# Kernel tuning notes

Measured on AMD Instinct MI355X. Metric: run time of the kernel, lower is better.

The kernel has to match this reference:

```python
import jax, jax.numpy as jnp
import numpy as np

N = 100_000   # nodes
E = 3_200_000 # edges
F = 13        # input features
H = 64        # hidden dim
G = 512       # graphs in batch
C = 2         # output classes
BN_EPS = 1e-5


def _linear(key, fan_in, fan_out):
    kw, kb = jax.random.split(key)
    bound = 1.0 / np.sqrt(fan_in)
    W = jax.random.uniform(kw, (fan_in, fan_out), jnp.float32, -bound, bound)
    b = jax.random.uniform(kb, (fan_out,), jnp.float32, -bound, bound)
    return W, b


def _conv_params(key, fin, fout):
    k1, k2, k3 = jax.random.split(key, 3)
    W1, b1 = _linear(k1, fin, fout)
    W2, b2 = _linear(k2, fout, fout)
    gamma = jnp.ones((fout,), jnp.float32)
    beta = jnp.zeros((fout,), jnp.float32)
    mean = jax.random.normal(k3, (fout,), jnp.float32) * 0.1
    var = jnp.ones((fout,), jnp.float32)
    return W1, b1, gamma, beta, mean, var, W2, b2


def setup_inputs() -> dict:
    key = jax.random.key(0)
    ks = jax.random.split(key, 10)
    x = jax.random.normal(ks[0], (N, F), jnp.float32)
    src = jax.random.randint(ks[1], (E,), 0, N, jnp.int32)
    dst = jax.random.randint(ks[2], (E,), 0, N, jnp.int32)
    batch = jnp.sort(jax.random.randint(ks[3], (N,), 0, G, jnp.int32))
    inp = {"x": x, "src": src, "dst": dst, "batch": batch}
    for i, name in enumerate(["c1", "c2", "c3"]):
        fin = F if i == 0 else H
        W1, b1, g, be, m, v, W2, b2 = _conv_params(ks[4 + i], fin, H)
        inp.update({f"{name}_W1": W1, f"{name}_b1": b1, f"{name}_g": g,
                    f"{name}_be": be, f"{name}_m": m, f"{name}_v": v,
                    f"{name}_W2": W2, f"{name}_b2": b2})
    inp["fc1_W"], inp["fc1_b"] = _linear(ks[7], 3 * H, 3 * H)
    inp["fc2_W"], inp["fc2_b"] = _linear(ks[8], 3 * H, C)
    return inp


def _mlp(h, W1, b1, g, be, m, v, W2, b2):
    # Linear -> BatchNorm1d (inference, running stats) -> ReLU -> Linear -> ReLU
    h = h @ W1 + b1
    h = (h - m) * jax.lax.rsqrt(v + BN_EPS) * g + be
    h = jax.nn.relu(h)
    return jax.nn.relu(h @ W2 + b2)


def _gin_conv(x, src, dst, mlp_params):
    # GINConv with eps=0: MLP(x + sum_{j->i} x_j) via scatter-add over edges
    agg = jax.ops.segment_sum(x[src], dst, num_segments=N)
    return _mlp(x + agg, *mlp_params)


def reference(x, src, dst, batch,
              c1_W1, c1_b1, c1_g, c1_be, c1_m, c1_v, c1_W2, c1_b2,
              c2_W1, c2_b1, c2_g, c2_be, c2_m, c2_v, c2_W2, c2_b2,
              c3_W1, c3_b1, c3_g, c3_be, c3_m, c3_v, c3_W2, c3_b2,
              fc1_W, fc1_b, fc2_W, fc2_b):
    h1 = jax.nn.relu(_gin_conv(x, src, dst, (c1_W1, c1_b1, c1_g, c1_be, c1_m, c1_v, c1_W2, c1_b2)))
    h2 = jax.nn.relu(_gin_conv(h1, src, dst, (c2_W1, c2_b1, c2_g, c2_be, c2_m, c2_v, c2_W2, c2_b2)))
    h3 = jax.nn.relu(_gin_conv(h2, src, dst, (c3_W1, c3_b1, c3_g, c3_be, c3_m, c3_v, c3_W2, c3_b2)))
    p1 = jax.ops.segment_sum(h1, batch, num_segments=G)
    p2 = jax.ops.segment_sum(h2, batch, num_segments=G)
    p3 = jax.ops.segment_sum(h3, batch, num_segments=G)
    h = jnp.concatenate([p1, p2, p3], axis=1)  # [G, 3H]
    h = jax.nn.relu(h @ fc1_W + fc1_b)
    # Dropout is identity in eval mode
    h = h @ fc2_W + fc2_b
    return jax.nn.log_softmax(h, axis=-1)
```

## Files before the change

### kernel.cpp

```cpp
#include <hip/hip_runtime.h>

#define NNODES 100000
#define NEDGES 3200000
#define NF 13
#define NFP 16
#define NG 512
#define BN_EPS 1e-5f
#define NTILES (NNODES / 16)
#define CAP 72

#define BSH 9
#define NBUCK ((NNODES + 511) / 512)
#define RCAP 18500
#define PTILE 4096
#define NPBLK ((NEDGES + PTILE - 1) / PTILE)
#define CVTB 200

#define NCHUNK ((NNODES + 63) / 64)
#define NPTASK (3 * NCHUNK)

typedef __attribute__((ext_vector_type(8))) _Float16 f16x8;
typedef __attribute__((ext_vector_type(4))) _Float16 f16x4;
typedef __attribute__((ext_vector_type(4))) float f32x4;

__device__ __forceinline__ unsigned short f2h(float f) {
    union { _Float16 h; unsigned short u; } c;
    c.h = (_Float16)f;
    return c.u;
}
__device__ __forceinline__ float h2f(unsigned short u) {
    union { _Float16 h; unsigned short u; } c;
    c.u = u;
    return (float)c.h;
}

__device__ __forceinline__ f16x8 shfl_xor8(f16x8 v, int m) {
    union { f16x8 h; int i[4]; } a, b;
    a.h = v;
#pragma unroll
    for (int k = 0; k < 4; ++k) b.i[k] = __shfl_xor(a.i[k], m, 64);
    return b.h;
}
__device__ __forceinline__ f16x4 shfl_xor4(f16x4 v, int m) {
    union { f16x4 h; int i[2]; } a, b;
    a.h = v;
#pragma unroll
    for (int k = 0; k < 2; ++k) b.i[k] = __shfl_xor(a.i[k], m, 64);
    return b.h;
}

__launch_bounds__(256)
__global__ void prep_kernel(const int* __restrict__ src, const int* __restrict__ dst,
                            int* __restrict__ gcount, int* __restrict__ pairbuf,
                            const float* __restrict__ x, unsigned short* __restrict__ xh,
                            const float* __restrict__ w10, const float* __restrict__ w20,
                            const float* __restrict__ w11, const float* __restrict__ w21,
                            const float* __restrict__ w12, const float* __restrict__ w22,
                            unsigned short* __restrict__ wfrag) {
    __shared__ int lhist[NBUCK];
    __shared__ int lbase[NBUCK];
    __shared__ int lpos[NBUCK];
    int bid = blockIdx.x;
    int t = threadIdx.x;

    if (bid < NPBLK) {
        int base = bid * PTILE;
        int cnt = NEDGES - base; if (cnt > PTILE) cnt = PTILE;
        int v[PTILE / 256], b[PTILE / 256];
#pragma unroll
        for (int j = 0; j < PTILE / 256; ++j) {
            int i = t + j * 256;
            if (i < cnt) {
                int d = __builtin_nontemporal_load(dst + base + i);
                int s = __builtin_nontemporal_load(src + base + i);
                b[j] = d >> BSH;
                v[j] = ((d & 511) << 17) | s;
            } else b[j] = -1;
        }
        if (t < NBUCK) lhist[t] = 0;
        __syncthreads();
#pragma unroll
        for (int j = 0; j < PTILE / 256; ++j)
            if (b[j] >= 0) atomicAdd(&lhist[b[j]], 1);
        __syncthreads();
        if (t < NBUCK) {
            lbase[t] = atomicAdd(&gcount[t], lhist[t]);
            lpos[t] = 0;
        }
        __syncthreads();
#pragma unroll
        for (int j = 0; j < PTILE / 256; ++j) {
            if (b[j] >= 0) {
                int p = atomicAdd(&lpos[b[j]], 1);
                pairbuf[(size_t)b[j] * RCAP + lbase[b[j]] + p] = v[j];
            }
        }
    } else if (bid < NPBLK + 12) {
        int tid = (bid - NPBLK) * 256 + t;
        if (tid >= 3072) return;
        int layer = tid >> 10;
        int rem = tid & 1023;
        int mat = rem >> 9;
        int tile = (rem >> 7) & 3;
        int chunk = (rem >> 6) & 1;
        int lane = rem & 63;
        int quad = lane >> 4, n = lane & 15;
        const float* W = (layer == 0) ? (mat ? w20 : w10)
                       : (layer == 1) ? (mat ? w21 : w11)
                                      : (mat ? w22 : w12);
        int K = (layer == 0 && mat == 0) ? NF : 64;
        unsigned short* o = wfrag + ((size_t)tid) * 8;
#pragma unroll
        for (int j = 0; j < 8; ++j) {
            int k = chunk * 32 + quad * 8 + j;
            float val = (k < K) ? W[k * 64 + tile * 16 + n] : 0.f;
            o[j] = f2h(val);
        }
    } else {
        const int total = NNODES * NFP;
        int idx = (bid - NPBLK - 12) * 256 + t;
        int stride = CVTB * 256;
        for (int i = idx; i < total; i += stride) {
            int n = i >> 4;
            int f = i & 15;
            xh[i] = (f < NF) ? f2h(__builtin_nontemporal_load(x + n * NF + f))
                             : (unsigned short)0;
        }
    }
}

__launch_bounds__(512)
__global__ void bucket_scatter_kernel(const int* __restrict__ pairbuf,
                                      const int* __restrict__ gcount,
                                      int* __restrict__ cursor, int* __restrict__ csr) {
    __shared__ int lcnt[512];
    int bk = blockIdx.x;
    int lo = bk << BSH;
    int cnt = gcount[bk];
    if (threadIdx.x < 512) lcnt[threadIdx.x] = 0;
    __syncthreads();
    const int* pb = pairbuf + (size_t)bk * RCAP;
    for (int i = threadIdx.x; i < cnt; i += 512) {
        int p = __builtin_nontemporal_load(pb + i);
        int s = p & 0x1FFFF;
        int dl = p >> 17;
        int pos = atomicAdd(&lcnt[dl], 1);
        csr[(size_t)(lo + dl) * CAP + pos] = s;
    }
    __syncthreads();
    int n = lo + threadIdx.x;
    if (threadIdx.x < 512 && n < NNODES) cursor[n] = n * CAP + lcnt[threadIdx.x];
}

template <int LAYER>
__launch_bounds__(256, 6)
__global__ void gin_layer_kernel(const unsigned short* __restrict__ xin,
                                 const int* __restrict__ cursor,
                                 const int* __restrict__ csr,
                                 const unsigned short* __restrict__ wfrag,
                                 const float* __restrict__ b1, const float* __restrict__ gam,
                                 const float* __restrict__ be, const float* __restrict__ mu,
                                 const float* __restrict__ var, const float* __restrict__ b2,
                                 unsigned short* __restrict__ hout) {
    constexpr int FSTR = (LAYER == 1) ? NFP : 64;
    __shared__ __align__(16) unsigned short ytile[16][80];
    __shared__ __align__(16) unsigned short ztile[16][80];
    int lane = threadIdx.x & 63;
    int wid = threadIdx.x >> 6;
    int quad = lane >> 4, n16 = lane & 15;
    int nb = blockIdx.x * 16;

    if constexpr (LAYER == 1) {
        int g = lane >> 2;
        int r = lane & 3;
#pragma unroll
        for (int pp = 0; pp < 2; ++pp) {
            int lnA = wid * 4 + pp * 2;
            int nA = nb + lnA, nB = nA + 1;
            int jA = nA * CAP, jB = nB * CAP;
            int endA = __builtin_nontemporal_load(cursor + nA);
            int endB = __builtin_nontemporal_load(cursor + nB);
            f16x4 accA = {0, 0, 0, 0};
            f16x4 accB = {0, 0, 0, 0};
            if (g == 0) {
                accA = *(const f16x4*)&xin[(size_t)nA * FSTR + r * 4];
                accB = *(const f16x4*)&xin[(size_t)nB * FSTR + r * 4];
            }
            while (jA + 16 <= endA && jB + 16 <= endB) {
                int iA = __builtin_nontemporal_load(csr + jA + g);
                int iB = __builtin_nontemporal_load(csr + jB + g);
                f16x4 vA = *(const f16x4*)&xin[(size_t)iA * FSTR + r * 4];
                f16x4 vB = *(const f16x4*)&xin[(size_t)iB * FSTR + r * 4];
                accA += vA; accB += vB;
                jA += 16; jB += 16;
            }
            for (; jA + 32 <= endA; jA += 32) {
                int i0 = __builtin_nontemporal_load(csr + jA + g);
                int i1 = __builtin_nontemporal_load(csr + jA + 16 + g);
                f16x4 v0 = *(const f16x4*)&xin[(size_t)i0 * FSTR + r * 4];
                f16x4 v1 = *(const f16x4*)&xin[(size_t)i1 * FSTR + r * 4];
                accA += v0; accA += v1;
            }
            for (; jA < endA; jA += 16) {
                int e = jA + g;
                if (e < endA) {
                    int i0 = __builtin_nontemporal_load(csr + e);
                    accA += *(const f16x4*)&xin[(size_t)i0 * FSTR + r * 4];
                }
            }
            for (; jB + 32 <= endB; jB += 32) {
                int i0 = __builtin_nontemporal_load(csr + jB + g);
                int i1 = __builtin_nontemporal_load(csr + jB + 16 + g);
                f16x4 v0 = *(const f16x4*)&xin[(size_t)i0 * FSTR + r * 4];
                f16x4 v1 = *(const f16x4*)&xin[(size_t)i1 * FSTR + r * 4];
                accB += v0; accB += v1;
            }
            for (; jB < endB; jB += 16) {
                int e = jB + g;
                if (e < endB) {
                    int i0 = __builtin_nontemporal_load(csr + e);
                    accB += *(const f16x4*)&xin[(size_t)i0 * FSTR + r * 4];
                }
            }
#pragma unroll
            for (int m = 4; m < 64; m <<= 1) {
                accA += shfl_xor4(accA, m);
                accB += shfl_xor4(accB, m);
            }
            if (g == 0) {
                *(f16x4*)&ytile[lnA][r * 4] = accA;
                *(f16x4*)&ytile[lnA + 1][r * 4] = accB;
            } else if (g == 1) {
                f16x4 z = {0, 0, 0, 0};
                *(f16x4*)&ytile[lnA][16 + r * 4] = z;
                *(f16x4*)&ytile[lnA + 1][16 + r * 4] = z;
            }
        }
    } else {
        int g = lane >> 3;
        int r = lane & 7;
#pragma unroll
        for (int pp = 0; pp < 2; ++pp) {
            int lnA = wid * 4 + pp * 2;
            int nA = nb + lnA, nB = nA + 1;
            int jA = nA * CAP, jB = nB * CAP;
            int endA = __builtin_nontemporal_load(cursor + nA);
            int endB = __builtin_nontemporal_load(cursor + nB);
            f16x8 accA = {0, 0, 0, 0, 0, 0, 0, 0};
            f16x8 accB = {0, 0, 0, 0, 0, 0, 0, 0};
            if (g == 0) {
                accA = *(const f16x8*)&xin[(size_t)nA * 64 + r * 8];
                accB = *(const f16x8*)&xin[(size_t)nB * 64 + r * 8];
            }
            while (jA + 16 <= endA && jB + 16 <= endB) {
                int iA0 = __builtin_nontemporal_load(csr + jA + g);
                int iA1 = __builtin_nontemporal_load(csr + jA + 8 + g);
                int iB0 = __builtin_nontemporal_load(csr + jB + g);
                int iB1 = __builtin_nontemporal_load(csr + jB + 8 + g);
                f16x8 vA0 = *(const f16x8*)&xin[(size_t)iA0 * 64 + r * 8];
                f16x8 vA1 = *(const f16x8*)&xin[(size_t)iA1 * 64 + r * 8];
                f16x8 vB0 = *(const f16x8*)&xin[(size_t)iB0 * 64 + r * 8];
                f16x8 vB1 = *(const f16x8*)&xin[(size_t)iB1 * 64 + r * 8];
                accA += vA0; accA += vA1;
                accB += vB0; accB += vB1;
                jA += 16; jB += 16;
            }
            for (; jA + 16 <= endA; jA += 16) {
                int i0 = __builtin_nontemporal_load(csr + jA + g);
                int i1 = __builtin_nontemporal_load(csr + jA + 8 + g);
                f16x8 v0 = *(const f16x8*)&xin[(size_t)i0 * 64 + r * 8];
                f16x8 v1 = *(const f16x8*)&xin[(size_t)i1 * 64 + r * 8];
                accA += v0; accA += v1;
            }
            for (; jA < endA; jA += 8) {
                int e = jA + g;
                if (e < endA) {
                    int i0 = __builtin_nontemporal_load(csr + e);
                    accA += *(const f16x8*)&xin[(size_t)i0 * 64 + r * 8];
                }
            }
            for (; jB + 16 <= endB; jB += 16) {
                int i0 = __builtin_nontemporal_load(csr + jB + g);
                int i1 = __builtin_nontemporal_load(csr + jB + 8 + g);
                f16x8 v0 = *(const f16x8*)&xin[(size_t)i0 * 64 + r * 8];
                f16x8 v1 = *(const f16x8*)&xin[(size_t)i1 * 64 + r * 8];
                accB += v0; accB += v1;
            }
            for (; jB < endB; jB += 8) {
                int e = jB + g;
                if (e < endB) {
                    int i0 = __builtin_nontemporal_load(csr + e);
                    accB += *(const f16x8*)&xin[(size_t)i0 * 64 + r * 8];
                }
            }
#pragma unroll
            for (int m = 8; m < 64; m <<= 1) {
                accA += shfl_xor8(accA, m);
                accB += shfl_xor8(accB, m);
            }
            if (g == 0) {
                *(f16x8*)&ytile[lnA][r * 8] = accA;
                *(f16x8*)&ytile[lnA + 1][r * 8] = accB;
            }
        }
    }

    const f16x8* wf = (const f16x8*)wfrag;
    f16x8 w1f0 = wf[((0 * 4 + wid) * 2 + 0) * 64 + lane];
    f16x8 w1f1 = (LAYER == 2) ? wf[((0 * 4 + wid) * 2 + 1) * 64 + lane] : w1f0;
    f16x8 w2f0 = wf[((1 * 4 + wid) * 2 + 0) * 64 + lane];
    f16x8 w2f1 = wf[((1 * 4 + wid) * 2 + 1) * 64 + lane];
    int f = wid * 16 + n16;
    float sc = gam[f] * rsqrtf(var[f] + BN_EPS);
    float sh = (b1[f] - mu[f]) * sc + be[f];
    float bb2 = b2[f];

    __syncthreads();

    f16x8 a0 = *(const f16x8*)&ytile[n16][quad * 8];
    f32x4 z4 = {0.f, 0.f, 0.f, 0.f};
    z4 = __builtin_amdgcn_mfma_f32_16x16x32_f16(a0, w1f0, z4, 0, 0, 0);
    if constexpr (LAYER == 2) {
        f16x8 a1 = *(const f16x8*)&ytile[n16][32 + quad * 8];
        z4 = __builtin_amdgcn_mfma_f32_16x16x32_f16(a1, w1f1, z4, 0, 0, 0);
    }
#pragma unroll
    for (int reg = 0; reg < 4; ++reg) {
        float z = fmaxf(fmaf(z4[reg], sc, sh), 0.f);
        ztile[quad * 4 + reg][wid * 16 + n16] = f2h(z);
    }
    __syncthreads();

    f16x8 az0 = *(const f16x8*)&ztile[n16][quad * 8];
    f16x8 az1 = *(const f16x8*)&ztile[n16][32 + quad * 8];
    f32x4 h4 = {0.f, 0.f, 0.f, 0.f};
    h4 = __builtin_amdgcn_mfma_f32_16x16x32_f16(az0, w2f0, h4, 0, 0, 0);
    h4 = __builtin_amdgcn_mfma_f32_16x16x32_f16(az1, w2f1, h4, 0, 0, 0);
#pragma unroll
    for (int reg = 0; reg < 4; ++reg) {
        float h = fmaxf(h4[reg] + bb2, 0.f);
        hout[(size_t)(nb + quad * 4 + reg) * 64 + wid * 16 + n16] = f2h(h);
    }
}

__launch_bounds__(256)
__global__ void pool_kernel(const unsigned short* __restrict__ h1,
                            const unsigned short* __restrict__ h2,
                            const unsigned short* __restrict__ h3,
                            const int* __restrict__ batch,
                            float* __restrict__ pool) {
    int task = blockIdx.x * 4 + (threadIdx.x >> 6);
    if (task >= NPTASK) return;
    int lane = threadIdx.x & 63;
    int layer = task / NCHUNK;
    int c = task - layer * NCHUNK;
    int n0 = c * 64;
    int n1 = n0 + 64; if (n1 > NNODES) n1 = NNODES;
    const unsigned short* hb = (layer == 0) ? h1 : (layer == 1) ? h2 : h3;
    float acc = 0.f;
    int curg = batch[n0];
    for (int n = n0; n < n1; ++n) {
        int gid = batch[n];
        if (gid != curg) {
            atomicAdd(&pool[(size_t)curg * 192 + layer * 64 + lane], acc);
            acc = 0.f;
            curg = gid;
        }
        acc += h2f(__builtin_nontemporal_load(hb + (size_t)n * 64 + lane));
    }
    atomicAdd(&pool[(size_t)curg * 192 + layer * 64 + lane], acc);
}

__global__ void head_kernel(const float* __restrict__ pool,
                            const float* __restrict__ fc1W, const float* __restrict__ fc1b,
                            const float* __restrict__ fc2W, const float* __restrict__ fc2b,
                            float* __restrict__ out) {
    __shared__ float ps[192];
    __shared__ float hs[192];
    int gi = blockIdx.x;
    int t = threadIdx.x;
    ps[t] = pool[gi * 192 + t];
    __syncthreads();
    float acc = fc1b[t];
#pragma unroll 8
    for (int k = 0; k < 192; ++k) acc = fmaf(ps[k], fc1W[k * 192 + t], acc);
    hs[t] = fmaxf(acc, 0.f);
    __syncthreads();
    if (t == 0) {
        float l0 = fc2b[0], l1 = fc2b[1];
        for (int k = 0; k < 192; ++k) {
            float h = hs[k];
            l0 = fmaf(h, fc2W[k * 2 + 0], l0);
            l1 = fmaf(h, fc2W[k * 2 + 1], l1);
        }
        float mx = fmaxf(l0, l1);
        float lse = mx + logf(expf(l0 - mx) + expf(l1 - mx));
        out[gi * 2 + 0] = l0 - lse;
        out[gi * 2 + 1] = l1 - lse;
    }
}

extern "C" void kernel_launch(void* const* d_in, const int* in_sizes, int n_in,
                              void* d_out, int out_size, void* d_ws, size_t ws_size,
                              hipStream_t stream) {
    const float* x = (const float*)d_in[0];
    const int* src = (const int*)d_in[1];
    const int* dst = (const int*)d_in[2];
    const int* batch = (const int*)d_in[3];
    const float* c1[8];
    const float* c2[8];
    const float* c3[8];
    for (int i = 0; i < 8; ++i) {
        c1[i] = (const float*)d_in[4 + i];
        c2[i] = (const float*)d_in[12 + i];
        c3[i] = (const float*)d_in[20 + i];
    }
    const float* fc1W = (const float*)d_in[28];
    const float* fc1b = (const float*)d_in[29];
    const float* fc2W = (const float*)d_in[30];
    const float* fc2b = (const float*)d_in[31];
    float* out = (float*)d_out;

    unsigned short* base = (unsigned short*)d_ws;
    const size_t NA = (size_t)NNODES * 64;
    unsigned short* xh  = base;
    unsigned short* h1  = xh + (size_t)NNODES * NFP;
    unsigned short* h2  = h1 + NA;
    unsigned short* h3  = h2 + NA;
    unsigned short* wfrag = h3 + NA;
    float* pool = (float*)(wfrag + 3 * 8192);
    int* ibase = (int*)(pool + (size_t)NG * 192);
    int* cursor  = ibase;
    int* gcount  = ibase + NNODES;
    int* csr     = gcount + NBUCK;
    int* pairbuf = csr + (size_t)NNODES * CAP + 256;

    hipMemsetAsync(gcount, 0, NBUCK * sizeof(int), stream);
    hipMemsetAsync(pool, 0, (size_t)NG * 192 * sizeof(float), stream);

    prep_kernel<<<NPBLK + 12 + CVTB, 256, 0, stream>>>(
        src, dst, gcount, pairbuf, x, xh,
        c1[0], c1[6], c2[0], c2[6], c3[0], c3[6], wfrag);
    bucket_scatter_kernel<<<NBUCK, 512, 0, stream>>>(pairbuf, gcount, cursor, csr);

    gin_layer_kernel<1><<<NTILES, 256, 0, stream>>>(
        xh, cursor, csr, wfrag + 0 * 8192,
        c1[1], c1[2], c1[3], c1[4], c1[5], c1[7], h1);
    gin_layer_kernel<2><<<NTILES, 256, 0, stream>>>(
        h1, cursor, csr, wfrag + 1 * 8192,
        c2[1], c2[2], c2[3], c2[4], c2[5], c2[7], h2);
    gin_layer_kernel<2><<<NTILES, 256, 0, stream>>>(
        h2, cursor, csr, wfrag + 2 * 8192,
        c3[1], c3[2], c3[3], c3[4], c3[5], c3[7], h3);

    pool_kernel<<<(NPTASK + 3) / 4, 256, 0, stream>>>(h1, h2, h3, batch, pool);
    head_kernel<<<NG, 192, 0, stream>>>(pool, fc1W, fc1b, fc2W, fc2b, out);
}
```

Before: 407.7 us.

## Replace two-pass bucketed CSR build with direct global-atomic slot insertion

Removes the bucket histogram/pairbuf pass and the per-bucket scatter kernel, and builds the fixed-capacity adjacency directly with one global atomicAdd per edge on a per-node counter. The GIN layers now read the degree count and clamp it to CAP instead of reading a precomputed cursor. It also lowers the launch-bounds occupancy hint from 6 to 4 waves. This trades one kernel and an intermediate buffer for 3.2M scattered global atomics, and it silently drops any edges beyond CAP per node.

```diff
diff --git a/kernel.cpp b/kernel.cpp
--- a/kernel.cpp
+++ b/kernel.cpp
@@ -9,13 +9,6 @@
 #define NTILES (NNODES / 16)
 #define CAP 72
 
-#define BSH 9
-#define NBUCK ((NNODES + 511) / 512)
-#define RCAP 18500
-#define PTILE 4096
-#define NPBLK ((NEDGES + PTILE - 1) / PTILE)
-#define CVTB 200
-
 #define NCHUNK ((NNODES + 63) / 64)
 #define NPTASK (3 * NCHUNK)
 
@@ -50,53 +43,29 @@
 }
 
 __launch_bounds__(256)
-__global__ void prep_kernel(const int* __restrict__ src, const int* __restrict__ dst,
-                            int* __restrict__ gcount, int* __restrict__ pairbuf,
-                            const float* __restrict__ x, unsigned short* __restrict__ xh,
+__global__ void build_csr_kernel(const int* __restrict__ src, const int* __restrict__ dst,
+                                 int* __restrict__ cnt, int* __restrict__ csr) {
+    int idx = blockIdx.x * blockDim.x + threadIdx.x;
+    int stride = gridDim.x * blockDim.x;
+    for (int e = idx; e < NEDGES; e += stride) {
+        int d = __builtin_nontemporal_load(dst + e);
+        int s = __builtin_nontemporal_load(src + e);
+        int pos = atomicAdd(&cnt[d], 1);
+        if (pos < CAP) csr[(size_t)d * CAP + pos] = s;
+    }
+}
+
+#define CVTB 200
+__launch_bounds__(256)
+__global__ void prep_kernel(const float* __restrict__ x, unsigned short* __restrict__ xh,
                             const float* __restrict__ w10, const float* __restrict__ w20,
                             const float* __restrict__ w11, const float* __restrict__ w21,
                             const float* __restrict__ w12, const float* __restrict__ w22,
                             unsigned short* __restrict__ wfrag) {
-    __shared__ int lhist[NBUCK];
-    __shared__ int lbase[NBUCK];
-    __shared__ int lpos[NBUCK];
     int bid = blockIdx.x;
     int t = threadIdx.x;
-
-    if (bid < NPBLK) {
-        int base = bid * PTILE;
-        int cnt = NEDGES - base; if (cnt > PTILE) cnt = PTILE;
-        int v[PTILE / 256], b[PTILE / 256];
-#pragma unroll
-        for (int j = 0; j < PTILE / 256; ++j) {
-            int i = t + j * 256;
-            if (i < cnt) {
-                int d = __builtin_nontemporal_load(dst + base + i);
-                int s = __builtin_nontemporal_load(src + base + i);
-                b[j] = d >> BSH;
-                v[j] = ((d & 511) << 17) | s;
-            } else b[j] = -1;
-        }
-        if (t < NBUCK) lhist[t] = 0;
-        __syncthreads();
-#pragma unroll
-        for (int j = 0; j < PTILE / 256; ++j)
-            if (b[j] >= 0) atomicAdd(&lhist[b[j]], 1);
-        __syncthreads();
-        if (t < NBUCK) {
-            lbase[t] = atomicAdd(&gcount[t], lhist[t]);
-            lpos[t] = 0;
-        }
-        __syncthreads();
-#pragma unroll
-        for (int j = 0; j < PTILE / 256; ++j) {
-            if (b[j] >= 0) {
-                int p = atomicAdd(&lpos[b[j]], 1);
-                pairbuf[(size_t)b[j] * RCAP + lbase[b[j]] + p] = v[j];
-            }
-        }
-    } else if (bid < NPBLK + 12) {
-        int tid = (bid - NPBLK) * 256 + t;
+    if (bid < 12) {
+        int tid = bid * 256 + t;
         if (tid >= 3072) return;
         int layer = tid >> 10;
         int rem = tid & 1023;
@@ -118,7 +87,7 @@
         }
     } else {
         const int total = NNODES * NFP;
-        int idx = (bid - NPBLK - 12) * 256 + t;
+        int idx = (bid - 12) * 256 + t;
         int stride = CVTB * 256;
         for (int i = idx; i < total; i += stride) {
             int n = i >> 4;
@@ -129,33 +98,10 @@
     }
 }
 
-__launch_bounds__(512)
-__global__ void bucket_scatter_kernel(const int* __restrict__ pairbuf,
-                                      const int* __restrict__ gcount,
-                                      int* __restrict__ cursor, int* __restrict__ csr) {
-    __shared__ int lcnt[512];
-    int bk = blockIdx.x;
-    int lo = bk << BSH;
-    int cnt = gcount[bk];
-    if (threadIdx.x < 512) lcnt[threadIdx.x] = 0;
-    __syncthreads();
-    const int* pb = pairbuf + (size_t)bk * RCAP;
-    for (int i = threadIdx.x; i < cnt; i += 512) {
-        int p = __builtin_nontemporal_load(pb + i);
-        int s = p & 0x1FFFF;
-        int dl = p >> 17;
-        int pos = atomicAdd(&lcnt[dl], 1);
-        csr[(size_t)(lo + dl) * CAP + pos] = s;
-    }
-    __syncthreads();
-    int n = lo + threadIdx.x;
-    if (threadIdx.x < 512 && n < NNODES) cursor[n] = n * CAP + lcnt[threadIdx.x];
-}
-
 template <int LAYER>
-__launch_bounds__(256, 6)
+__launch_bounds__(256, 4)
 __global__ void gin_layer_kernel(const unsigned short* __restrict__ xin,
-                                 const int* __restrict__ cursor,
+                                 const int* __restrict__ cnt,
                                  const int* __restrict__ csr,
                                  const unsigned short* __restrict__ wfrag,
                                  const float* __restrict__ b1, const float* __restrict__ gam,
@@ -177,9 +123,12 @@
         for (int pp = 0; pp < 2; ++pp) {
             int lnA = wid * 4 + pp * 2;
             int nA = nb + lnA, nB = nA + 1;
+            int dA = __builtin_nontemporal_load(cnt + nA);
+            int dB = __builtin_nontemporal_load(cnt + nB);
+            if (dA > CAP) dA = CAP;
+            if (dB > CAP) dB = CAP;
             int jA = nA * CAP, jB = nB * CAP;
-            int endA = __builtin_nontemporal_load(cursor + nA);
-            int endB = __builtin_nontemporal_load(cursor + nB);
+            int endA = jA + dA, endB = jB + dB;
             f16x4 accA = {0, 0, 0, 0};
             f16x4 accB = {0, 0, 0, 0};
             if (g == 0) {
@@ -243,9 +192,12 @@
         for (int pp = 0; pp < 2; ++pp) {
             int lnA = wid * 4 + pp * 2;
             int nA = nb + lnA, nB = nA + 1;
+            int dA = __builtin_nontemporal_load(cnt + nA);
+            int dB = __builtin_nontemporal_load(cnt + nB);
+            if (dA > CAP) dA = CAP;
+            if (dB > CAP) dB = CAP;
             int jA = nA * CAP, jB = nB * CAP;
-            int endA = __builtin_nontemporal_load(cursor + nA);
-            int endB = __builtin_nontemporal_load(cursor + nB);
+            int endA = jA + dA, endB = jB + dB;
             f16x8 accA = {0, 0, 0, 0, 0, 0, 0, 0};
             f16x8 accB = {0, 0, 0, 0, 0, 0, 0, 0};
             if (g == 0) {
@@ -430,27 +382,24 @@
     unsigned short* wfrag = h3 + NA;
     float* pool = (float*)(wfrag + 3 * 8192);
     int* ibase = (int*)(pool + (size_t)NG * 192);
-    int* cursor  = ibase;
-    int* gcount  = ibase + NNODES;
-    int* csr     = gcount + NBUCK;
-    int* pairbuf = csr + (size_t)NNODES * CAP + 256;
-
-    hipMemsetAsync(gcount, 0, NBUCK * sizeof(int), stream);
+    int* cnt = ibase;
+    int* csr = cnt + NNODES;
+
+    hipMemsetAsync(cnt, 0, NNODES * sizeof(int), stream);
     hipMemsetAsync(pool, 0, (size_t)NG * 192 * sizeof(float), stream);
 
-    prep_kernel<<<NPBLK + 12 + CVTB, 256, 0, stream>>>(
-        src, dst, gcount, pairbuf, x, xh,
-        c1[0], c1[6], c2[0], c2[6], c3[0], c3[6], wfrag);
-    bucket_scatter_kernel<<<NBUCK, 512, 0, stream>>>(pairbuf, gcount, cursor, csr);
+    prep_kernel<<<12 + CVTB, 256, 0, stream>>>(
+        x, xh, c1[0], c1[6], c2[0], c2[6], c3[0], c3[6], wfrag);
+    build_csr_kernel<<<2048, 256, 0, stream>>>(src, dst, cnt, csr);
 
     gin_layer_kernel<1><<<NTILES, 256, 0, stream>>>(
-        xh, cursor, csr, wfrag + 0 * 8192,
+        xh, cnt, csr, wfrag + 0 * 8192,
         c1[1], c1[2], c1[3], c1[4], c1[5], c1[7], h1);
     gin_layer_kernel<2><<<NTILES, 256, 0, stream>>>(
-        h1, cursor, csr, wfrag + 1 * 8192,
+        h1, cnt, csr, wfrag + 1 * 8192,
         c2[1], c2[2], c2[3], c2[4], c2[5], c2[7], h2);
     gin_layer_kernel<2><<<NTILES, 256, 0, stream>>>(
-        h2, cursor, csr, wfrag + 2 * 8192,
+        h2, cnt, csr, wfrag + 2 * 8192,
         c3[1], c3[2], c3[3], c3[4], c3[5], c3[7], h3);
 
     pool_kernel<<<(NPTASK + 3) / 4, 256, 0, stream>>>(h1, h2, h3, batch, pool);
```

Result: slower. 611.1 us (+49.9%).

## Replace atomic global bucketing with per-block sort and per-bucket gather for CSR build

Applied to the files above, without the earlier changes.

Edge bucketing drops the global atomic counter and fixed-capacity per-bucket regions. Each block now sorts its edge tile locally by bucket in shared memory, writes the tile contiguously with vector nontemporal stores, and records a per-block segment table. A gather kernel then has one thread per source block walk that block's segment for its bucket and fill the CSR with shared-memory atomics, clamping to CAP. The intent is to remove the scattered global writes and the global atomic contention. The price is a serial per-thread loop in the gather, and the layer kernel's min-blocks hint also drops from 6 to 4.

```diff
diff --git a/kernel.cpp b/kernel.cpp
--- a/kernel.cpp
+++ b/kernel.cpp
@@ -11,10 +11,9 @@
 
 #define BSH 9
 #define NBUCK ((NNODES + 511) / 512)
-#define RCAP 18500
 #define PTILE 4096
 #define NPBLK ((NEDGES + PTILE - 1) / PTILE)
-#define CVTB 200
+#define EPT (PTILE / 256)
 
 #define NCHUNK ((NNODES + 63) / 64)
 #define NPTASK (3 * NCHUNK)
@@ -22,6 +21,7 @@
 typedef __attribute__((ext_vector_type(8))) _Float16 f16x8;
 typedef __attribute__((ext_vector_type(4))) _Float16 f16x4;
 typedef __attribute__((ext_vector_type(4))) float f32x4;
+typedef __attribute__((ext_vector_type(4))) int i32x4;
 
 __device__ __forceinline__ unsigned short f2h(float f) {
     union { _Float16 h; unsigned short u; } c;
@@ -50,53 +50,101 @@
 }
 
 __launch_bounds__(256)
-__global__ void prep_kernel(const int* __restrict__ src, const int* __restrict__ dst,
-                            int* __restrict__ gcount, int* __restrict__ pairbuf,
-                            const float* __restrict__ x, unsigned short* __restrict__ xh,
+__global__ void block_sort_kernel(const int* __restrict__ src, const int* __restrict__ dst,
+                                  int* __restrict__ pairout, int* __restrict__ bseg) {
+    __shared__ int hist[256];
+    __shared__ int scanbuf[256];
+    __shared__ int spair[PTILE];
+    int t = threadIdx.x;
+    int bid = blockIdx.x;
+    int base = bid * PTILE;
+    int cnt = NEDGES - base; if (cnt > PTILE) cnt = PTILE;
+
+    int v[EPT], b[EPT];
+#pragma unroll
+    for (int j = 0; j < EPT; ++j) {
+        int i = t + j * 256;
+        if (i < cnt) {
+            int d = __builtin_nontemporal_load(dst + base + i);
+            int s = __builtin_nontemporal_load(src + base + i);
+            b[j] = d >> BSH;
+            v[j] = ((d & 511) << 17) | s;
+        } else b[j] = -1;
+    }
+    hist[t] = 0;
+    __syncthreads();
+#pragma unroll
+    for (int j = 0; j < EPT; ++j)
+        if (b[j] >= 0) atomicAdd(&hist[b[j]], 1);
+    __syncthreads();
+    int val = hist[t];
+    scanbuf[t] = val;
+    __syncthreads();
+    for (int off = 1; off < 256; off <<= 1) {
+        int add = (t >= off) ? scanbuf[t - off] : 0;
+        __syncthreads();
+        scanbuf[t] += add;
+        __syncthreads();
+    }
+    int excl = scanbuf[t] - val;
+    if (t < NBUCK) bseg[(size_t)bid * NBUCK + t] = (excl << 13) | val;
+    hist[t] = excl;
+    __syncthreads();
+#pragma unroll
+    for (int j = 0; j < EPT; ++j) {
+        if (b[j] >= 0) {
+            int pos = atomicAdd(&hist[b[j]], 1);
+            spair[pos] = v[j];
+        }
+    }
+    __syncthreads();
+    const i32x4* sp4 = (const i32x4*)spair;
+    i32x4* po4 = (i32x4*)(pairout + (size_t)bid * PTILE);
+    for (int j = t; j < PTILE / 4; j += 256)
+        __builtin_nontemporal_store(sp4[j], po4 + j);
+}
+
+__launch_bounds__(512)
+__global__ void bucket_gather_kernel(const int* __restrict__ pairout,
+                                     const int* __restrict__ bseg,
+                                     int* __restrict__ cursor, int* __restrict__ csr) {
+    __shared__ int lcnt[512];
+    int bk = blockIdx.x;
+    int lo = bk << BSH;
+    int t = threadIdx.x;
+    lcnt[t] = 0;
+    __syncthreads();
+    for (int k = t; k < NPBLK; k += 512) {
+        int pk = bseg[(size_t)k * NBUCK + bk];
+        int cnt = pk & 8191;
+        const int* seg = pairout + (size_t)k * PTILE + (pk >> 13);
+        for (int i = 0; i < cnt; ++i) {
+            int p = __builtin_nontemporal_load(seg + i);
+            int dl = p >> 17;
+            int s = p & 0x1FFFF;
+            int pos = atomicAdd(&lcnt[dl], 1);
+            if (pos < CAP) csr[(size_t)(lo + dl) * CAP + pos] = s;
+        }
+    }
+    __syncthreads();
+    int n = lo + t;
+    if (n < NNODES) {
+        int d = lcnt[t]; if (d > CAP) d = CAP;
+        cursor[n] = n * CAP + d;
+    }
+}
+
+#define CVTB 200
+__launch_bounds__(256)
+__global__ void prep_kernel(const float* __restrict__ x, unsigned short* __restrict__ xh,
                             const float* __restrict__ w10, const float* __restrict__ w20,
                             const float* __restrict__ w11, const float* __restrict__ w21,
                             const float* __restrict__ w12, const float* __restrict__ w22,
                             unsigned short* __restrict__ wfrag) {
-    __shared__ int lhist[NBUCK];
-    __shared__ int lbase[NBUCK];
-    __shared__ int lpos[NBUCK];
     int bid = blockIdx.x;
     int t = threadIdx.x;
-
-    if (bid < NPBLK) {
-        int base = bid * PTILE;
-        int cnt = NEDGES - base; if (cnt > PTILE) cnt = PTILE;
-        int v[PTILE / 256], b[PTILE / 256];
-#pragma unroll
-        for (int j = 0; j < PTILE / 256; ++j) {
-            int i = t + j * 256;
-            if (i < cnt) {
-                int d = __builtin_nontemporal_load(dst + base + i);
-                int s = __builtin_nontemporal_load(src + base + i);
-                b[j] = d >> BSH;
-                v[j] = ((d & 511) << 17) | s;
-            } else b[j] = -1;
-        }
-        if (t < NBUCK) lhist[t] = 0;
-        __syncthreads();
-#pragma unroll
-        for (int j = 0; j < PTILE / 256; ++j)
-            if (b[j] >= 0) atomicAdd(&lhist[b[j]], 1);
-        __syncthreads();
-        if (t < NBUCK) {
-            lbase[t] = atomicAdd(&gcount[t], lhist[t]);
-            lpos[t] = 0;
-        }
-        __syncthreads();
-#pragma unroll
-        for (int j = 0; j < PTILE / 256; ++j) {
-            if (b[j] >= 0) {
-                int p = atomicAdd(&lpos[b[j]], 1);
-                pairbuf[(size_t)b[j] * RCAP + lbase[b[j]] + p] = v[j];
-            }
-        }
-    } else if (bid < NPBLK + 12) {
-        int tid = (bid - NPBLK) * 256 + t;
+    if (bid < 12) {
+        int tid = bid * 256 + t;
         if (tid >= 3072) return;
         int layer = tid >> 10;
         int rem = tid & 1023;
@@ -118,7 +166,7 @@
         }
     } else {
         const int total = NNODES * NFP;
-        int idx = (bid - NPBLK - 12) * 256 + t;
+        int idx = (bid - 12) * 256 + t;
         int stride = CVTB * 256;
         for (int i = idx; i < total; i += stride) {
             int n = i >> 4;
@@ -129,31 +177,8 @@
     }
 }
 
-__launch_bounds__(512)
-__global__ void bucket_scatter_kernel(const int* __restrict__ pairbuf,
-                                      const int* __restrict__ gcount,
-                                      int* __restrict__ cursor, int* __restrict__ csr) {
-    __shared__ int lcnt[512];
-    int bk = blockIdx.x;
-    int lo = bk << BSH;
-    int cnt = gcount[bk];
-    if (threadIdx.x < 512) lcnt[threadIdx.x] = 0;
-    __syncthreads();
-    const int* pb = pairbuf + (size_t)bk * RCAP;
-    for (int i = threadIdx.x; i < cnt; i += 512) {
-        int p = __builtin_nontemporal_load(pb + i);
-        int s = p & 0x1FFFF;
-        int dl = p >> 17;
-        int pos = atomicAdd(&lcnt[dl], 1);
-        csr[(size_t)(lo + dl) * CAP + pos] = s;
-    }
-    __syncthreads();
-    int n = lo + threadIdx.x;
-    if (threadIdx.x < 512 && n < NNODES) cursor[n] = n * CAP + lcnt[threadIdx.x];
-}
-
 template <int LAYER>
-__launch_bounds__(256, 6)
+__launch_bounds__(256, 4)
 __global__ void gin_layer_kernel(const unsigned short* __restrict__ xin,
                                  const int* __restrict__ cursor,
                                  const int* __restrict__ csr,
@@ -178,8 +203,7 @@
             int lnA = wid * 4 + pp * 2;
             int nA = nb + lnA, nB = nA + 1;
             int jA = nA * CAP, jB = nB * CAP;
-            int endA = __builtin_nontemporal_load(cursor + nA);
-            int endB = __builtin_nontemporal_load(cursor + nB);
+            int endA = cursor[nA], endB = cursor[nB];
             f16x4 accA = {0, 0, 0, 0};
             f16x4 accB = {0, 0, 0, 0};
             if (g == 0) {
@@ -244,8 +268,7 @@
             int lnA = wid * 4 + pp * 2;
             int nA = nb + lnA, nB = nA + 1;
             int jA = nA * CAP, jB = nB * CAP;
-            int endA = __builtin_nontemporal_load(cursor + nA);
-            int endB = __builtin_nontemporal_load(cursor + nB);
+            int endA = cursor[nA], endB = cursor[nB];
             f16x8 accA = {0, 0, 0, 0, 0, 0, 0, 0};
             f16x8 accB = {0, 0, 0, 0, 0, 0, 0, 0};
             if (g == 0) {
@@ -431,17 +454,16 @@
     float* pool = (float*)(wfrag + 3 * 8192);
     int* ibase = (int*)(pool + (size_t)NG * 192);
     int* cursor  = ibase;
-    int* gcount  = ibase + NNODES;
-    int* csr     = gcount + NBUCK;
-    int* pairbuf = csr + (size_t)NNODES * CAP + 256;
-
-    hipMemsetAsync(gcount, 0, NBUCK * sizeof(int), stream);
-    hipMemsetAsync(pool, 0, (size_t)NG * 192 * sizeof(float), stream);
-
-    prep_kernel<<<NPBLK + 12 + CVTB, 256, 0, stream>>>(
-        src, dst, gcount, pairbuf, x, xh,
-        c1[0], c1[6], c2[0], c2[6], c3[0], c3[6], wfrag);
-    bucket_scatter_kernel<<<NBUCK, 512, 0, stream>>>(pairbuf, gcount, cursor, csr);
+    int* csr     = cursor + NNODES;
+    int* pairout = csr + (size_t)NNODES * CAP + 256;
+    int* bseg    = pairout + (size_t)NPBLK * PTILE;
+
+    (void)hipMemsetAsync(pool, 0, (size_t)NG * 192 * sizeof(float), stream);
+
+    block_sort_kernel<<<NPBLK, 256, 0, stream>>>(src, dst, pairout, bseg);
+    prep_kernel<<<12 + CVTB, 256, 0, stream>>>(
+        x, xh, c1[0], c1[6], c2[0], c2[6], c3[0], c3[6], wfrag);
+    bucket_gather_kernel<<<NBUCK, 512, 0, stream>>>(pairout, bseg, cursor, csr);
 
     gin_layer_kernel<1><<<NTILES, 256, 0, stream>>>(
         xh, cursor, csr, wfrag + 0 * 8192,
```

After: 461.0 us. +13.1%, slower.
